# Performance work log

Hardware: AMD Instinct MI355X
Metric: run time of the kernel (lower is better)

The kernel has to match this reference:

```python
import jax, jax.numpy as jnp
import numpy as np

SIGMA1 = 0.1  # init kwarg s


def setup_inputs() -> dict:
    key = jax.random.key(0)
    k1, k2 = jax.random.split(key)
    N, D = 8192, 128
    fvec = jax.random.normal(k1, (N, D), dtype=jnp.float32)
    Lvec = jax.random.randint(k2, (N,), 0, 1024, dtype=jnp.int32)
    a = jnp.ones((), dtype=jnp.float32)
    return {"fvec": fvec, "Lvec": Lvec, "a": a, "IPC": 512, "bz": 8192}


def reference(fvec, Lvec, a, IPC, bz):
    # data != 'SOP' branch of HSELoss.forward (Lvec is unused on this path).
    N = fvec.shape[0]
    # F.normalize(fvec, p=2, dim=1) with eps clamp
    norm = jnp.maximum(jnp.linalg.norm(fvec, axis=1, keepdims=True), 1e-12)
    fn = fvec / norm
    # distMC: cosine-sim matmul with diagonal forced to -1
    idx = jnp.arange(N)
    Dist = (fn @ fn.T).at[idx, idx].set(-1.0)  # [N, N]

    Dd = jax.lax.stop_gradient(Dist)  # D_detach clones
    rows = idx[:, None]
    cols = idx[None, :]
    row_sel = (rows >= bz - IPC) & (rows < bz)
    # easy: mask cols [2*IPC, bz) on the last IPC rows
    easy = jnp.where(row_sel & (cols >= 2 * IPC) & (cols < bz), -1.0, Dd)
    # hard: mask cols [0, 2*IPC) and [bz-IPC, bz) on the last IPC rows
    hard_cols = (cols < 2 * IPC) | ((cols >= bz - IPC) & (cols < bz))
    hard = jnp.where(row_sel & hard_cols, -1.0, Dd)

    I_easy = jnp.argmax(easy, axis=1)  # first max index, matches torch .max(1)
    I_hard = jnp.argmax(hard, axis=1)
    VCE = Dist[idx, I_easy]
    VCH = Dist[idx, I_hard]
    T1 = jnp.stack([VCE, VCH], axis=1)[-IPC:]  # [IPC, 2]
    Prob1 = -jax.nn.log_softmax(T1 / SIGMA1, axis=1)[:, 0]
    return a * Prob1.mean()
```

## Files before the change

kernel.cpp:

```cpp
#include <hip/hip_runtime.h>
#include <hip/hip_bf16.h>
#include <math.h>

constexpr int N   = 8192;
constexpr int D   = 128;
constexpr int IPC = 512;
constexpr int BZ  = 8192;
constexpr int Q0  = BZ - IPC;
constexpr int NQ  = IPC;
constexpr int JMAX = BZ - IPC;
constexpr int JBLK = 128;
constexpr int NJB  = JMAX / JBLK;
constexpr int EASY_JB = (2 * IPC) / JBLK;
constexpr int QBLK = 64;
constexpr int NQB  = NQ / QBLK;
constexpr int RSTR = 136;

typedef __attribute__((ext_vector_type(8))) short short8;
typedef __attribute__((ext_vector_type(4))) float f32x4;

__global__ __launch_bounds__(256) void kmain(const float* __restrict__ f,
                                             float* __restrict__ pm) {
    __shared__ __align__(16) short S[192 * RSTR];
    __shared__ float red[4][QBLK];

    const int tid  = threadIdx.x;
    const int lane = tid & 63;
    const int wv   = tid >> 6;
    const int jblk = blockIdx.x;
    const int qblk = blockIdx.y;

    {
        const int sub = tid & 15;
        const int rof = tid >> 4;
        #pragma unroll
        for (int i = 0; i < 12; ++i) {
            int ridx = i * 16 + rof;
            int grow = (ridx < QBLK) ? (Q0 + qblk * QBLK + ridx)
                                     : (jblk * JBLK + (ridx - QBLK));
            const float* rp = f + (size_t)grow * D + sub * 8;
            float4 v0 = *(const float4*)(rp);
            float4 v1 = *(const float4*)(rp + 4);
            float ss = v0.x*v0.x + v0.y*v0.y + v0.z*v0.z + v0.w*v0.w
                     + v1.x*v1.x + v1.y*v1.y + v1.z*v1.z + v1.w*v1.w;
            #pragma unroll
            for (int off = 1; off < 16; off <<= 1) ss += __shfl_xor(ss, off, 64);
            float r = 1.0f / fmaxf(sqrtf(ss), 1e-12f);
            float sc[8] = { v0.x*r, v0.y*r, v0.z*r, v0.w*r,
                            v1.x*r, v1.y*r, v1.z*r, v1.w*r };
            short8 h;
            #pragma unroll
            for (int e = 0; e < 8; ++e) {
                __hip_bfloat16 b = __float2bfloat16(sc[e]);
                h[e] = *(short*)&b;
            }
            *(short8*)&S[ridx * RSTR + sub * 8] = h;
        }
    }
    __syncthreads();

    const int row16 = lane & 15;
    const int kgrp  = lane >> 4;
    const short* As = S;
    const short* Bs = S + QBLK * RSTR + wv * 32 * RSTR;

    f32x4 acc[4][2] = {};
    #pragma unroll
    for (int c = 0; c < 4; ++c) {
        const int ko = c * 32 + kgrp * 8;
        short8 a[4], b[2];
        #pragma unroll
        for (int g = 0; g < 4; ++g)
            a[g] = *(const short8*)(As + (g * 16 + row16) * RSTR + ko);
        #pragma unroll
        for (int t = 0; t < 2; ++t)
            b[t] = *(const short8*)(Bs + (t * 16 + row16) * RSTR + ko);
        #pragma unroll
        for (int g = 0; g < 4; ++g)
            #pragma unroll
            for (int t = 0; t < 2; ++t)
                acc[g][t] = __builtin_amdgcn_mfma_f32_16x16x32_bf16(a[g], b[t], acc[g][t], 0, 0, 0);
    }

    float vg[4][4];
    #pragma unroll
    for (int g = 0; g < 4; ++g)
        #pragma unroll
        for (int r = 0; r < 4; ++r)
            vg[g][r] = fmaxf(acc[g][0][r], acc[g][1][r]);
    #pragma unroll
    for (int off = 1; off < 16; off <<= 1)
        #pragma unroll
        for (int g = 0; g < 4; ++g)
            #pragma unroll
            for (int r = 0; r < 4; ++r)
                vg[g][r] = fmaxf(vg[g][r], __shfl_xor(vg[g][r], off, 64));

    if ((lane & 15) == 0) {
        int sgrp = lane >> 4;
        #pragma unroll
        for (int g = 0; g < 4; ++g)
            #pragma unroll
            for (int r = 0; r < 4; ++r)
                red[wv][g * 16 + sgrp * 4 + r] = vg[g][r];
    }
    __syncthreads();
    if (tid < QBLK) {
        float m = fmaxf(fmaxf(red[0][tid], red[1][tid]),
                        fmaxf(red[2][tid], red[3][tid]));
        pm[(size_t)(qblk * QBLK + tid) * NJB + jblk] = m;
    }
}

__global__ __launch_bounds__(512) void kfinal(const float* __restrict__ pm,
                                              const float* __restrict__ a_in,
                                              float* __restrict__ out) {
    __shared__ float wsum[8];
    int q = threadIdx.x;
    const float* row = pm + (size_t)q * NJB;
    float vce = -1e30f, vch = -1e30f;
    #pragma unroll
    for (int c = 0; c < EASY_JB; ++c) vce = fmaxf(vce, row[c]);
    #pragma unroll
    for (int c = EASY_JB; c < NJB; ++c) vch = fmaxf(vch, row[c]);
    float d = (vch - vce) * 10.0f;
    float p = (d > 0.0f) ? (d + log1pf(expf(-d))) : log1pf(expf(d));
    #pragma unroll
    for (int off = 32; off > 0; off >>= 1) p += __shfl_xor(p, off, 64);
    int lane = q & 63, w = q >> 6;
    if (lane == 0) wsum[w] = p;
    __syncthreads();
    if (q == 0) {
        float s = 0.0f;
        #pragma unroll
        for (int i = 0; i < 8; ++i) s += wsum[i];
        out[0] = a_in[0] * (s / (float)NQ);
    }
}

extern "C" void kernel_launch(void* const* d_in, const int* in_sizes, int n_in,
                              void* d_out, int out_size, void* d_ws, size_t ws_size,
                              hipStream_t stream) {
    const float* f = (const float*)d_in[0];
    const float* a = (const float*)d_in[2];

    float* pm  = (float*)d_ws;
    float* out = (float*)d_out;

    dim3 g(NJB, NQB);
    kmain<<<g, 256, 0, stream>>>(f, pm);
    kfinal<<<1, 512, 0, stream>>>(pm, a, out);
}
```

Baseline: 71.48 us.

## Fuse final reduction into main kernel via atomic max and last-block pattern

Each block now folds its per-row partial maxima straight into two global arrays (easy and hard) using atomicMax on order-preserving encoded floats, replacing the per-block partial-max buffer. A global counter finds the last block to finish, and that block computes the softmax loss and writes the output, so the separate reduction kernel goes away. A small init kernel is added to zero the workspace. This trades one kernel launch and the strided partial-max reads for contended atomics and an extra tiny launch.

```diff
diff --git a/kernel.cpp b/kernel.cpp
--- a/kernel.cpp
+++ b/kernel.cpp
@@ -14,15 +14,36 @@
 constexpr int EASY_JB = (2 * IPC) / JBLK;
 constexpr int QBLK = 64;
 constexpr int NQB  = NQ / QBLK;
+constexpr int NBLK = NJB * NQB;
 constexpr int RSTR = 136;
+constexpr int WSWORDS = 64 + 2 * NQ;
 
 typedef __attribute__((ext_vector_type(8))) short short8;
 typedef __attribute__((ext_vector_type(4))) float f32x4;
 
+__device__ __forceinline__ unsigned enc_f32(float f) {
+    unsigned b = __float_as_uint(f);
+    return (b & 0x80000000u) ? ~b : (b | 0x80000000u);
+}
+__device__ __forceinline__ float dec_f32(unsigned u) {
+    unsigned b = (u & 0x80000000u) ? (u ^ 0x80000000u) : ~u;
+    return __uint_as_float(b);
+}
+
+__global__ __launch_bounds__(1024) void kinit(unsigned* __restrict__ ws) {
+    int t = threadIdx.x;
+    ws[t] = 0u;
+    if (t < WSWORDS - 1024) ws[1024 + t] = 0u;
+}
+
 __global__ __launch_bounds__(256) void kmain(const float* __restrict__ f,
-                                             float* __restrict__ pm) {
+                                             unsigned* __restrict__ ws,
+                                             const float* __restrict__ a_in,
+                                             float* __restrict__ out) {
     __shared__ __align__(16) short S[192 * RSTR];
     __shared__ float red[4][QBLK];
+    __shared__ float wsum[8];
+    __shared__ int lastflag;
 
     const int tid  = threadIdx.x;
     const int lane = tid & 63;
@@ -105,32 +126,41 @@
                 red[wv][g * 16 + sgrp * 4 + r] = vg[g][r];
     }
     __syncthreads();
+
+    unsigned* keys = ws + 64;
     if (tid < QBLK) {
         float m = fmaxf(fmaxf(red[0][tid], red[1][tid]),
                         fmaxf(red[2][tid], red[3][tid]));
-        pm[(size_t)(qblk * QBLK + tid) * NJB + jblk] = m;
+        unsigned* dst = keys + (jblk < EASY_JB ? 0 : NQ) + qblk * QBLK + tid;
+        atomicMax(dst, enc_f32(m));
     }
-}
+    __threadfence();
+    __syncthreads();
 
-__global__ __launch_bounds__(512) void kfinal(const float* __restrict__ pm,
-                                              const float* __restrict__ a_in,
-                                              float* __restrict__ out) {
-    __shared__ float wsum[8];
-    int q = threadIdx.x;
-    const float* row = pm + (size_t)q * NJB;
-    float vce = -1e30f, vch = -1e30f;
+    if (tid == 0) {
+        unsigned prev = atomicAdd(ws, 1u);
+        lastflag = (prev == (unsigned)(NBLK - 1));
+    }
+    __syncthreads();
+    if (!lastflag) return;
+
+    __threadfence();
     #pragma unroll
-    for (int c = 0; c < EASY_JB; ++c) vce = fmaxf(vce, row[c]);
-    #pragma unroll
-    for (int c = EASY_JB; c < NJB; ++c) vch = fmaxf(vch, row[c]);
-    float d = (vch - vce) * 10.0f;
-    float p = (d > 0.0f) ? (d + log1pf(expf(-d))) : log1pf(expf(d));
-    #pragma unroll
-    for (int off = 32; off > 0; off >>= 1) p += __shfl_xor(p, off, 64);
-    int lane = q & 63, w = q >> 6;
-    if (lane == 0) wsum[w] = p;
+    for (int half = 0; half < 2; ++half) {
+        int q = half * 256 + tid;
+        unsigned ue = __hip_atomic_load(&keys[q],      __ATOMIC_RELAXED, __HIP_MEMORY_SCOPE_AGENT);
+        unsigned uh = __hip_atomic_load(&keys[NQ + q], __ATOMIC_RELAXED, __HIP_MEMORY_SCOPE_AGENT);
+        float vce = dec_f32(ue);
+        float vch = dec_f32(uh);
+        float d = (vch - vce) * 10.0f;
+        float p = (d > 0.0f) ? (d + log1pf(expf(-d))) : log1pf(expf(d));
+        #pragma unroll
+        for (int off = 32; off > 0; off >>= 1) p += __shfl_xor(p, off, 64);
+        int l = tid & 63, w = tid >> 6;
+        if (l == 0) wsum[half * 4 + w] = p;
+    }
     __syncthreads();
-    if (q == 0) {
+    if (tid == 0) {
         float s = 0.0f;
         #pragma unroll
         for (int i = 0; i < 8; ++i) s += wsum[i];
@@ -144,10 +174,11 @@
     const float* f = (const float*)d_in[0];
     const float* a = (const float*)d_in[2];
 
-    float* pm  = (float*)d_ws;
-    float* out = (float*)d_out;
+    unsigned* ws  = (unsigned*)d_ws;
+    float*    out = (float*)d_out;
+
+    kinit<<<1, 1024, 0, stream>>>(ws);
 
     dim3 g(NJB, NQB);
-    kmain<<<g, 256, 0, stream>>>(f, pm);
-    kfinal<<<1, 512, 0, stream>>>(pm, a, out);
+    kmain<<<g, 256, 0, stream>>>(f, ws, a, out);
 }
```

New measurement: 99.57 us. 39.3% more time.
